# Kernel optimization log

Measured on AMD Instinct MI355X. Metric: run time of the kernel, lower is better.

## Reference

```python
import jax, jax.numpy as jnp
import numpy as np

DIM = 384
HEADS = 12
WS = (7, 7, 7)
N = WS[0] * WS[1] * WS[2]  # 343
NW = 64   # number of windows (mask dim)
B_ = 64   # num_windows * batch
CPB_HIDDEN = 512


def _make_buffers():
    # relative coords table: (1, 2Wd-1, 2Wh-1, 2Ww-1, 3), log-spaced per Swin-V2
    axes = [np.arange(-(w - 1), w, dtype=np.float32) / (w - 1) for w in WS]
    g = np.stack(np.meshgrid(*axes, indexing='ij'), axis=-1)[None]  # (1,13,13,13,3)
    g = g * 8.0
    table = np.sign(g) * np.log2(np.abs(g) + 1.0) / np.log2(8.0)
    # relative position index: (N, N) int
    coords = np.stack(np.meshgrid(*[np.arange(w) for w in WS], indexing='ij'))  # (3,Wd,Wh,Ww)
    cf = coords.reshape(3, -1)
    rel = (cf[:, :, None] - cf[:, None, :]).transpose(1, 2, 0).astype(np.int64)  # (N,N,3)
    rel[..., 0] += WS[0] - 1
    rel[..., 1] += WS[1] - 1
    rel[..., 2] += WS[2] - 1
    rel[..., 0] *= (2 * WS[1] - 1) * (2 * WS[2] - 1)
    rel[..., 1] *= 2 * WS[2] - 1
    idx = rel.sum(-1)
    return jnp.asarray(table, dtype=jnp.float32), jnp.asarray(idx, dtype=jnp.int32)


def setup_inputs() -> dict:
    key = jax.random.key(0)
    ks = jax.random.split(key, 10)
    table, idx = _make_buffers()
    return {
        'x': jax.random.normal(ks[0], (B_, N, DIM), dtype=jnp.float32),
        'mask': jax.random.normal(ks[1], (NW, N, N), dtype=jnp.float32),
        'qkv_w': jax.random.normal(ks[2], (3 * DIM, DIM), dtype=jnp.float32) * 0.02,
        'q_bias': jax.random.normal(ks[3], (DIM,), dtype=jnp.float32) * 0.02,
        'v_bias': jax.random.normal(ks[4], (DIM,), dtype=jnp.float32) * 0.02,
        'logit_scale': jnp.log(10.0 * jnp.ones((HEADS, 1, 1), dtype=jnp.float32)),
        'cpb_w1': jax.random.normal(ks[5], (CPB_HIDDEN, 3), dtype=jnp.float32) * 0.02,
        'cpb_b1': jax.random.normal(ks[6], (CPB_HIDDEN,), dtype=jnp.float32) * 0.02,
        'cpb_w2': jax.random.normal(ks[7], (HEADS, CPB_HIDDEN), dtype=jnp.float32) * 0.02,
        'proj_w': jax.random.normal(ks[8], (DIM, DIM), dtype=jnp.float32) * 0.02,
        'proj_b': jax.random.normal(ks[9], (DIM,), dtype=jnp.float32) * 0.02,
        'rel_table': table,
        'rel_index': idx,
    }


def reference(x, mask, qkv_w, q_bias, v_bias, logit_scale, cpb_w1, cpb_b1,
              cpb_w2, proj_w, proj_b, rel_table, rel_index):
    Bw, n, C = x.shape
    H = logit_scale.shape[0]
    hd = C // H
    qkv_bias = jnp.concatenate([q_bias, jnp.zeros_like(v_bias), v_bias])
    qkv = x @ qkv_w.T + qkv_bias                      # (Bw, n, 3C)
    qkv = qkv.reshape(Bw, n, 3, H, hd).transpose(2, 0, 3, 1, 4)
    q, k, v = qkv[0], qkv[1], qkv[2]                  # (Bw, H, n, hd)
    qn = q / jnp.clip(jnp.linalg.norm(q, axis=-1, keepdims=True), 1e-12)
    kn = k / jnp.clip(jnp.linalg.norm(k, axis=-1, keepdims=True), 1e-12)
    attn = jnp.einsum('bhnd,bhmd->bhnm', qn, kn)
    scale = jnp.exp(jnp.minimum(logit_scale, jnp.log(100.0)))  # clamp max log(1/0.01)
    attn = attn * scale
    # CPB MLP bias: (1,13,13,13,3) -> (table_size, H), gathered to (H, n, n)
    hidden = jax.nn.relu(rel_table @ cpb_w1.T + cpb_b1)
    bias_table = (hidden @ cpb_w2.T).reshape(-1, H)
    bias = bias_table[rel_index.reshape(-1)].reshape(n, n, H).transpose(2, 0, 1)
    bias = 16.0 * jax.nn.sigmoid(bias)
    attn = attn + bias[None]
    nW = mask.shape[0]
    attn = attn.reshape(Bw // nW, nW, H, n, n) + mask[None, :, None]
    attn = attn.reshape(Bw, H, n, n)
    attn = jax.nn.softmax(attn, axis=-1)
    out = jnp.einsum('bhnm,bhmd->bnhd', attn, v).reshape(Bw, n, C)
    out = out @ proj_w.T + proj_b
    return out
```

## Files before the change

### kernel.cpp

```cpp
#include <hip/hip_runtime.h>
#include <hip/hip_bf16.h>
#include <stdint.h>


typedef __attribute__((ext_vector_type(4))) float f32x4;
typedef __attribute__((ext_vector_type(8))) short short8;

#define DIM   384
#define HEADS 12
#define NTOK  343
#define NPAD  352
#define BW    64
#define MROWS (BW*NTOK)
#define MPAD  22016
#define NN    (NTOK*NTOK)
#define BPAD  352
#define LOG2E 1.44269504089f

__device__ __forceinline__ unsigned short f2bf(float f) {
  unsigned u = __float_as_uint(f);
  u += 0x7FFF + ((u >> 16) & 1);
  return (unsigned short)(u >> 16);
}

__device__ __forceinline__ void gload_lds16(const void* g, void* l) {
  __builtin_amdgcn_global_load_lds(
      (const __attribute__((address_space(1))) void*)g,
      (__attribute__((address_space(3))) void*)l, 16, 0, 0);
}

__global__ __launch_bounds__(256) void cvt_bf16(const float* __restrict__ in,
                                                unsigned short* __restrict__ out,
                                                long nvalid, long ntotal) {
  long i = ((long)blockIdx.x * 256 + threadIdx.x) * 8;
  if (i >= ntotal) return;
  short8 o;
  if (i < nvalid) {
    const float4* p = (const float4*)(in + i);
    float4 a = p[0], b = p[1];
    o[0] = (short)f2bf(a.x); o[1] = (short)f2bf(a.y);
    o[2] = (short)f2bf(a.z); o[3] = (short)f2bf(a.w);
    o[4] = (short)f2bf(b.x); o[5] = (short)f2bf(b.y);
    o[6] = (short)f2bf(b.z); o[7] = (short)f2bf(b.w);
  } else {
    o = (short8)0;
  }
  *(short8*)(out + i) = o;
}

__global__ __launch_bounds__(64) void cpb_tab(const float* __restrict__ tbl,
                                              const float* __restrict__ w1,
                                              const float* __restrict__ b1,
                                              const float* __restrict__ w2,
                                              float* __restrict__ btab) {
  const int r = blockIdx.x, lane = threadIdx.x;
  const float t0 = tbl[r*3], t1 = tbl[r*3+1], t2 = tbl[r*3+2];
  float acc[12];
#pragma unroll
  for (int hh = 0; hh < 12; ++hh) acc[hh] = 0.f;
  for (int u = 0; u < 8; ++u) {
    const int j = lane * 8 + u;
    const float hd = fmaxf(w1[j*3]*t0 + w1[j*3+1]*t1 + w1[j*3+2]*t2 + b1[j], 0.f);
#pragma unroll
    for (int hh = 0; hh < 12; ++hh) acc[hh] += hd * w2[hh*512 + j];
  }
#pragma unroll
  for (int hh = 0; hh < 12; ++hh) {
    float v = acc[hh];
    for (int msk = 1; msk < 64; msk <<= 1) v += __shfl_xor(v, msk);
    if (lane == 0) btab[r*12 + hh] = v;
  }
}

__global__ __launch_bounds__(256) void bias_gather(const float* __restrict__ btab,
                                                   const int* __restrict__ ridx,
                                                   float* __restrict__ bfull) {
  const int blk = blockIdx.x;
  const int hh = blk / NTOK, i = blk % NTOK;
  for (int j = threadIdx.x; j < BPAD; j += 256) {
    float o = 0.f;
    if (j < NTOK) {
      const int idx = ridx[i*NTOK + j];
      const float v = btab[idx*12 + hh];
      o = LOG2E * 16.f / (1.f + __expf(-v));
    }
    bfull[(size_t)blk*BPAD + j] = o;
  }
}

template<int MODE>
__global__ __launch_bounds__(256, 2) void gemm_k(
    const unsigned short* __restrict__ A, const unsigned short* __restrict__ B,
    unsigned short* __restrict__ o_qn, unsigned short* __restrict__ o_kn,
    unsigned short* __restrict__ o_vT,
    const float* __restrict__ q_bias, const float* __restrict__ v_bias,
    const float* __restrict__ lsc,
    float* __restrict__ o_out, const float* __restrict__ proj_b) {
  __shared__ alignas(16) uint8_t lds[32768];
  const int tid = threadIdx.x, wave = tid >> 6, lane = tid & 63;
  const int row0 = blockIdx.x * 128, col0 = blockIdx.y * 128;
  const int wm = wave & 1, wn = wave >> 1;
  const int l15 = lane & 15, lq = lane >> 4;
  f32x4 acc[4][4];
#pragma unroll
  for (int i = 0; i < 4; ++i)
#pragma unroll
    for (int j = 0; j < 4; ++j) acc[i][j] = (f32x4)0.f;

  const int stg_row = wave * 8 + (lane >> 3);
  const int srcblk = (lane & 7) ^ (lane >> 3);

  for (int kt = 0; kt < 6; ++kt) {
    const int k0 = kt * 64;
#pragma unroll
    for (int c = 0; c < 4; ++c) {
      const int row = c * 32 + stg_row;
      gload_lds16(A + (size_t)(row0 + row) * DIM + k0 + srcblk * 8,
                  lds + c * 4096 + wave * 1024);
      gload_lds16(B + (size_t)(col0 + row) * DIM + k0 + srcblk * 8,
                  lds + 16384 + c * 4096 + wave * 1024);
    }
    __syncthreads();
#pragma unroll
    for (int s = 0; s < 2; ++s) {
      short8 af[4], bfr[4];
#pragma unroll
      for (int i = 0; i < 4; ++i) {
        const int r = wm * 64 + i * 16 + l15;
        af[i] = *(const short8*)(lds + r * 128 + (((s * 4) | lq) ^ (r & 7)) * 16);
        const int cc = wn * 64 + i * 16 + l15;
        bfr[i] = *(const short8*)(lds + 16384 + cc * 128 + (((s * 4) | lq) ^ (cc & 7)) * 16);
      }
#pragma unroll
      for (int i = 0; i < 4; ++i)
#pragma unroll
        for (int j = 0; j < 4; ++j)
          acc[i][j] = __builtin_amdgcn_mfma_f32_16x16x32_bf16(af[i], bfr[j], acc[i][j], 0, 0, 0);
    }
    __syncthreads();
  }

  if (MODE == 0) {
#pragma unroll
    for (int i = 0; i < 4; ++i) {
      const int gr0 = row0 + wm * 64 + i * 16 + lq * 4;
#pragma unroll
      for (int p = 0; p < 2; ++p) {
        f32x4 c0 = acc[i][2 * p], c1 = acc[i][2 * p + 1];
        const int gcb = col0 + wn * 64 + p * 32;
        const int which = gcb / DIM, rem = gcb % DIM, hh = rem / 32;
        float b0 = 0.f, b1 = 0.f;
        if (which == 0) { b0 = q_bias[rem + l15]; b1 = q_bias[rem + l15 + 16]; }
        else if (which == 2) { b0 = v_bias[rem + l15]; b1 = v_bias[rem + l15 + 16]; }
#pragma unroll
        for (int r = 0; r < 4; ++r) { c0[r] += b0; c1[r] += b1; }
        float mult[4] = {1.f, 1.f, 1.f, 1.f};
        if (which < 2) {
          f32x4 ss;
#pragma unroll
          for (int r = 0; r < 4; ++r) ss[r] = c0[r] * c0[r] + c1[r] * c1[r];
#pragma unroll
          for (int msk = 1; msk < 16; msk <<= 1) {
#pragma unroll
            for (int r = 0; r < 4; ++r) ss[r] += __shfl_xor(ss[r], msk);
          }
          float sc = 1.f;
          if (which == 0)
            sc = __expf(fminf(lsc[hh], 4.6051701860f)) * LOG2E;
#pragma unroll
          for (int r = 0; r < 4; ++r) mult[r] = sc / fmaxf(sqrtf(ss[r]), 1e-12f);
        }
#pragma unroll
        for (int r = 0; r < 4; ++r) {
          const int gr = gr0 + r;
          if (gr >= MROWS) continue;
          const int b = gr / NTOK, nt = gr % NTOK;
          const unsigned short v0 = f2bf(c0[r] * mult[r]);
          const unsigned short v1 = f2bf(c1[r] * mult[r]);
          if (which == 0) {
            const size_t base = ((size_t)(b * HEADS + hh) * NTOK + nt) * 32 + l15;
            o_qn[base] = v0; o_qn[base + 16] = v1;
          } else if (which == 1) {
            const size_t base = ((size_t)(b * HEADS + hh) * NTOK + nt) * 32 + l15;
            o_kn[base] = v0; o_kn[base + 16] = v1;
          } else {
            const size_t base = ((size_t)(b * HEADS + hh) * 32 + l15) * NPAD + nt;
            o_vT[base] = v0; o_vT[base + (size_t)16 * NPAD] = v1;
          }
        }
      }
    }
  } else {
#pragma unroll
    for (int i = 0; i < 4; ++i) {
      const int gr0 = row0 + wm * 64 + i * 16 + lq * 4;
#pragma unroll
      for (int j = 0; j < 4; ++j) {
        const int gc = col0 + wn * 64 + j * 16 + l15;
        const float pb = proj_b[gc];
#pragma unroll
        for (int r = 0; r < 4; ++r) {
          const int gr = gr0 + r;
          if (gr < MROWS) o_out[(size_t)gr * DIM + gc] = acc[i][j][r] + pb;
        }
      }
    }
  }
}

__global__ __launch_bounds__(256, 3) void attn_k(
    const unsigned short* __restrict__ qn, const unsigned short* __restrict__ kn,
    const unsigned short* __restrict__ vT, const float* __restrict__ bfull,
    const float* __restrict__ mask, unsigned short* __restrict__ out1) {
  __shared__ alignas(16) uint8_t lds[33280];
  const int g = blockIdx.x;
  const int b = (g & 7) * 8 + (g >> 3) / HEADS;
  const int hh = (g >> 3) % HEADS;
  const int bh = b * HEADS + hh;
  const int tid = threadIdx.x;

  for (int r = tid; r < NPAD; r += 256) {
    uint4* dst = (uint4*)(lds + r * 80);
    if (r < NTOK) {
      const uint4* src = (const uint4*)(kn + ((size_t)bh * NTOK + r) * 32);
      dst[0] = src[0]; dst[1] = src[1]; dst[2] = src[2]; dst[3] = src[3];
    } else {
      uint4 z = make_uint4(0, 0, 0, 0);
      dst[0] = z; dst[1] = z; dst[2] = z; dst[3] = z;
    }
  }
  __syncthreads();

  const int wave = tid >> 6, lane = tid & 63;
  const int l15 = lane & 15, lq = lane >> 4;
  uint8_t* pbuf = lds + 28160 + wave * 1280;

  const unsigned short* vrow0 = vT + ((size_t)bh * 32 + l15) * NPAD;
  const unsigned short* vrow1 = vT + ((size_t)bh * 32 + 16 + l15) * NPAD;

  for (int qt = wave; qt < 22; qt += 4) {
    const int q0 = qt * 16;
    const int qc = min(q0 + l15, NTOK - 1);
    const short8 aq = *(const short8*)(qn + ((size_t)bh * NTOK + qc) * 32 + lq * 8);
    const float* brow = bfull + ((size_t)hh * NTOK + qc) * BPAD;
    const float* mrow = mask + (size_t)b * NN + (size_t)qc * NTOK;

    f32x4 o0 = (f32x4)0.f, o1 = (f32x4)0.f;
    float m_run = -1e30f, l_run = 0.f;

    f32x4 pf_ba[2], pf_bb[2];
    float pf_ma[2][4], pf_mb[2][4];
    short8 pf_v0[2], pf_v1[2], pf_k0[2], pf_k1[2];

    pf_ba[0] = *(const f32x4*)(brow + lq * 4);
    pf_bb[0] = *(const f32x4*)(brow + 16 + lq * 4);
#pragma unroll
    for (int r = 0; r < 4; ++r) {
      pf_ma[0][r] = mrow[lq * 4 + r];
      pf_mb[0][r] = mrow[16 + lq * 4 + r];
    }
    pf_v0[0] = *(const short8*)(vrow0 + lq * 8);
    pf_v1[0] = *(const short8*)(vrow1 + lq * 8);
    pf_k0[0] = *(const short8*)(lds + (l15) * 80 + lq * 16);
    pf_k1[0] = *(const short8*)(lds + (16 + l15) * 80 + lq * 16);

#pragma unroll
    for (int c = 0; c < 11; ++c) {
      const int cur = c & 1, nxt = cur ^ 1;
      if (c < 10) {
        const int kc = (c + 1) * 32;
        pf_ba[nxt] = *(const f32x4*)(brow + kc + lq * 4);
        pf_bb[nxt] = *(const f32x4*)(brow + kc + 16 + lq * 4);
#pragma unroll
        for (int r = 0; r < 4; ++r) {
          pf_ma[nxt][r] = mrow[kc + lq * 4 + r];
          const int kk = kc + 16 + lq * 4 + r;
          pf_mb[nxt][r] = mrow[(c == 9 && kk >= NTOK) ? 0 : kk];
        }
        pf_v0[nxt] = *(const short8*)(vrow0 + kc + lq * 8);
        pf_v1[nxt] = *(const short8*)(vrow1 + kc + lq * 8);
        pf_k0[nxt] = *(const short8*)(lds + (kc + l15) * 80 + lq * 16);
        pf_k1[nxt] = *(const short8*)(lds + (kc + 16 + l15) * 80 + lq * 16);
      }
      f32x4 s0 = __builtin_amdgcn_mfma_f32_16x16x32_bf16(pf_k0[cur], aq, (f32x4)0.f, 0, 0, 0);
      f32x4 s1 = __builtin_amdgcn_mfma_f32_16x16x32_bf16(pf_k1[cur], aq, (f32x4)0.f, 0, 0, 0);
#pragma unroll
      for (int r = 0; r < 4; ++r) {
        s0[r] = s0[r] + pf_ba[cur][r] + pf_ma[cur][r] * LOG2E;
        s1[r] = s1[r] + pf_bb[cur][r] + pf_mb[cur][r] * LOG2E;
      }
      if (c == 10) {
#pragma unroll
        for (int r = 0; r < 4; ++r)
          if (336 + lq * 4 + r >= NTOK) s1[r] = -1e30f;
      }
      float mx = fmaxf(fmaxf(fmaxf(s0[0], s0[1]), fmaxf(s0[2], s0[3])),
                       fmaxf(fmaxf(s1[0], s1[1]), fmaxf(s1[2], s1[3])));
      mx = fmaxf(mx, __shfl_xor(mx, 16));
      mx = fmaxf(mx, __shfl_xor(mx, 32));
      const float mn = fmaxf(m_run, mx);
      const float f = exp2f(m_run - mn);
      m_run = mn;
      float p0[4], p1[4], psum = 0.f;
#pragma unroll
      for (int r = 0; r < 4; ++r) {
        p0[r] = exp2f(s0[r] - mn);
        p1[r] = exp2f(s1[r] - mn);
        psum += p0[r] + p1[r];
      }
      l_run = l_run * f + psum;
      float fr[4];
#pragma unroll
      for (int r = 0; r < 4; ++r) fr[r] = __shfl(f, lq * 4 + r);
#pragma unroll
      for (int r = 0; r < 4; ++r) { o0[r] *= fr[r]; o1[r] *= fr[r]; }
      const unsigned uu0 = ((unsigned)f2bf(p0[1]) << 16) | f2bf(p0[0]);
      const unsigned uu1 = ((unsigned)f2bf(p0[3]) << 16) | f2bf(p0[2]);
      const unsigned uu2 = ((unsigned)f2bf(p1[1]) << 16) | f2bf(p1[0]);
      const unsigned uu3 = ((unsigned)f2bf(p1[3]) << 16) | f2bf(p1[2]);
      uint2* w0 = (uint2*)(pbuf + l15 * 80 + lq * 8);
      uint2* w1 = (uint2*)(pbuf + l15 * 80 + 32 + lq * 8);
      *w0 = make_uint2(uu0, uu1);
      *w1 = make_uint2(uu2, uu3);
      const short8 pfrag = *(const short8*)(pbuf + l15 * 80 + lq * 16);
      o0 = __builtin_amdgcn_mfma_f32_16x16x32_bf16(pfrag, pf_v0[cur], o0, 0, 0, 0);
      o1 = __builtin_amdgcn_mfma_f32_16x16x32_bf16(pfrag, pf_v1[cur], o1, 0, 0, 0);
    }
    l_run += __shfl_xor(l_run, 16);
    l_run += __shfl_xor(l_run, 32);
    const float invl = 1.f / l_run;
    float ir[4];
#pragma unroll
    for (int r = 0; r < 4; ++r) ir[r] = __shfl(invl, lq * 4 + r);
#pragma unroll
    for (int r = 0; r < 4; ++r) {
      const int q = q0 + lq * 4 + r;
      if (q < NTOK) {
        const size_t base = ((size_t)b * NTOK + q) * DIM + hh * 32 + l15;
        out1[base]      = f2bf(o0[r] * ir[r]);
        out1[base + 16] = f2bf(o1[r] * ir[r]);
      }
    }
  }
}

extern "C" void kernel_launch(void* const* d_in, const int* in_sizes, int n_in,
                              void* d_out, int out_size, void* d_ws, size_t ws_size,
                              hipStream_t stream) {
  const float* x      = (const float*)d_in[0];
  const float* mask   = (const float*)d_in[1];
  const float* qkv_w  = (const float*)d_in[2];
  const float* q_bias = (const float*)d_in[3];
  const float* v_bias = (const float*)d_in[4];
  const float* lsc    = (const float*)d_in[5];
  const float* cpb_w1 = (const float*)d_in[6];
  const float* cpb_b1 = (const float*)d_in[7];
  const float* cpb_w2 = (const float*)d_in[8];
  const float* proj_w = (const float*)d_in[9];
  const float* proj_b = (const float*)d_in[10];
  const float* rtab   = (const float*)d_in[11];
  const int*   ridx   = (const int*)d_in[12];
  float* out = (float*)d_out;
  uint8_t* ws = (uint8_t*)d_ws;

  size_t o = 0;
  auto alloc = [&](size_t bytes) { size_t r = o; o += (bytes + 255) & ~(size_t)255; return r; };
  const size_t off_xb  = alloc((size_t)MPAD * DIM * 2);
  const size_t off_qwb = alloc((size_t)1152 * DIM * 2);
  const size_t off_pwb = alloc((size_t)DIM * DIM * 2);
  const size_t off_qnb = alloc((size_t)BW * HEADS * NTOK * 32 * 2);
  const size_t off_knb = alloc((size_t)BW * HEADS * NTOK * 32 * 2);
  const size_t off_vTb = alloc((size_t)BW * HEADS * 32 * NPAD * 2);
  const size_t off_btab  = alloc((size_t)2197 * 12 * 4);
  const size_t off_bfull = alloc((size_t)HEADS * NTOK * BPAD * 4);
  (void)in_sizes; (void)n_in; (void)out_size;

  if (ws_size < o) {
    hipMemsetAsync(d_out, 0, (size_t)out_size * 4, stream);
    return;
  }

  unsigned short* xb  = (unsigned short*)(ws + off_xb);
  unsigned short* o1b = xb;
  unsigned short* qwb = (unsigned short*)(ws + off_qwb);
  unsigned short* pwb = (unsigned short*)(ws + off_pwb);
  unsigned short* qnb = (unsigned short*)(ws + off_qnb);
  unsigned short* knb = (unsigned short*)(ws + off_knb);
  unsigned short* vTb = (unsigned short*)(ws + off_vTb);
  float* btab  = (float*)(ws + off_btab);
  float* bfull = (float*)(ws + off_bfull);

  cvt_bf16<<<(long)MPAD * DIM / 8 / 256, 256, 0, stream>>>(x, xb, (long)MROWS * DIM, (long)MPAD * DIM);
  cvt_bf16<<<1152 * DIM / 8 / 256, 256, 0, stream>>>(qkv_w, qwb, 1152L * DIM, 1152L * DIM);
  cvt_bf16<<<DIM * DIM / 8 / 256, 256, 0, stream>>>(proj_w, pwb, (long)DIM * DIM, (long)DIM * DIM);
  cpb_tab<<<2197, 64, 0, stream>>>(rtab, cpb_w1, cpb_b1, cpb_w2, btab);
  bias_gather<<<HEADS * NTOK, 256, 0, stream>>>(btab, ridx, bfull);
  gemm_k<0><<<dim3(MPAD / 128, 1152 / 128), 256, 0, stream>>>(
      xb, qwb, qnb, knb, vTb, q_bias, v_bias, lsc, nullptr, nullptr);
  attn_k<<<BW * HEADS, 256, 0, stream>>>(qnb, knb, vTb, bfull, mask, o1b);
  gemm_k<1><<<dim3(MPAD / 128, DIM / 128), 256, 0, stream>>>(
      o1b, pwb, nullptr, nullptr, nullptr, nullptr, nullptr, nullptr, out, proj_b);
}
```

Baseline: 310.6 us.

## Replace online softmax with fixed-max exponent, split query tiles across two blocks

The attention kernel drops the running-max online softmax. It relies on a static upper bound: the cosine logits are bounded by the clamped scale, the bias is at most 16, and the shift SMAX is folded into the gathered bias table, so the exponent is computed directly without max reductions, shuffles or accumulator rescaling. Padding columns are masked through a -1e9 bias entry instead of a separate branch. Each (window, head) is split across two blocks to double the grid, occupancy is raised to 4 blocks per CU, and the P·V MFMA is software-pipelined one chunk behind using a double P buffer. Bf16 packing switches to truncation instead of round-to-nearest. The fixed max assumes the mask values are bounded; large mask values could overflow or underflow exp2.

```diff
diff --git a/kernel.cpp b/kernel.cpp
--- a/kernel.cpp
+++ b/kernel.cpp
@@ -16,11 +16,16 @@
 #define NN    (NTOK*NTOK)
 #define BPAD  352
 #define LOG2E 1.44269504089f
+#define SMAX  48.0f
 
 __device__ __forceinline__ unsigned short f2bf(float f) {
   unsigned u = __float_as_uint(f);
   u += 0x7FFF + ((u >> 16) & 1);
   return (unsigned short)(u >> 16);
+}
+
+__device__ __forceinline__ unsigned pk2bf(float lo, float hi) {
+  return (__float_as_uint(hi) & 0xFFFF0000u) | (__float_as_uint(lo) >> 16);
 }
 
 __device__ __forceinline__ void gload_lds16(const void* g, void* l) {
@@ -78,11 +83,11 @@
   const int blk = blockIdx.x;
   const int hh = blk / NTOK, i = blk % NTOK;
   for (int j = threadIdx.x; j < BPAD; j += 256) {
-    float o = 0.f;
+    float o = -1e9f;
     if (j < NTOK) {
       const int idx = ridx[i*NTOK + j];
       const float v = btab[idx*12 + hh];
-      o = LOG2E * 16.f / (1.f + __expf(-v));
+      o = LOG2E * 16.f / (1.f + __expf(-v)) - SMAX;
     }
     bfull[(size_t)blk*BPAD + j] = o;
   }
@@ -208,14 +213,16 @@
   }
 }
 
-__global__ __launch_bounds__(256, 3) void attn_k(
+__global__ __launch_bounds__(256, 4) void attn_k(
     const unsigned short* __restrict__ qn, const unsigned short* __restrict__ kn,
     const unsigned short* __restrict__ vT, const float* __restrict__ bfull,
     const float* __restrict__ mask, unsigned short* __restrict__ out1) {
-  __shared__ alignas(16) uint8_t lds[33280];
+  __shared__ alignas(16) uint8_t lds[38400];
   const int g = blockIdx.x;
-  const int b = (g & 7) * 8 + (g >> 3) / HEADS;
-  const int hh = (g >> 3) % HEADS;
+  const int idx = g >> 3;
+  const int b = (g & 7) * 8 + idx / 24;
+  const int r24 = idx % 24;
+  const int hh = r24 >> 1, half = r24 & 1;
   const int bh = b * HEADS + hh;
   const int tid = threadIdx.x;
 
@@ -233,98 +240,78 @@
 
   const int wave = tid >> 6, lane = tid & 63;
   const int l15 = lane & 15, lq = lane >> 4;
-  uint8_t* pbuf = lds + 28160 + wave * 1280;
+  uint8_t* pb0 = lds + 28160 + wave * 2560;
+  uint8_t* pb1 = pb0 + 1280;
 
   const unsigned short* vrow0 = vT + ((size_t)bh * 32 + l15) * NPAD;
   const unsigned short* vrow1 = vT + ((size_t)bh * 32 + 16 + l15) * NPAD;
 
-  for (int qt = wave; qt < 22; qt += 4) {
-    const int q0 = qt * 16;
+  for (int t = wave; t < 11; t += 4) {
+    const int q0 = (half * 11 + t) * 16;
     const int qc = min(q0 + l15, NTOK - 1);
     const short8 aq = *(const short8*)(qn + ((size_t)bh * NTOK + qc) * 32 + lq * 8);
     const float* brow = bfull + ((size_t)hh * NTOK + qc) * BPAD;
     const float* mrow = mask + (size_t)b * NN + (size_t)qc * NTOK;
 
     f32x4 o0 = (f32x4)0.f, o1 = (f32x4)0.f;
-    float m_run = -1e30f, l_run = 0.f;
-
-    f32x4 pf_ba[2], pf_bb[2];
-    float pf_ma[2][4], pf_mb[2][4];
-    short8 pf_v0[2], pf_v1[2], pf_k0[2], pf_k1[2];
-
-    pf_ba[0] = *(const f32x4*)(brow + lq * 4);
-    pf_bb[0] = *(const f32x4*)(brow + 16 + lq * 4);
+    float l_run = 0.f;
+
+    f32x4 pbA[2], pbB[2];
+    float pmA[2][4], pmB[2][4];
+    short8 kf0[2], kf1[2], vf0[2], vf1[2];
+
+    pbA[0] = *(const f32x4*)(brow + lq * 4);
+    pbB[0] = *(const f32x4*)(brow + 16 + lq * 4);
 #pragma unroll
     for (int r = 0; r < 4; ++r) {
-      pf_ma[0][r] = mrow[lq * 4 + r];
-      pf_mb[0][r] = mrow[16 + lq * 4 + r];
-    }
-    pf_v0[0] = *(const short8*)(vrow0 + lq * 8);
-    pf_v1[0] = *(const short8*)(vrow1 + lq * 8);
-    pf_k0[0] = *(const short8*)(lds + (l15) * 80 + lq * 16);
-    pf_k1[0] = *(const short8*)(lds + (16 + l15) * 80 + lq * 16);
-
-#pragma unroll
-    for (int c = 0; c < 11; ++c) {
+      pmA[0][r] = mrow[lq * 4 + r];
+      pmB[0][r] = mrow[16 + lq * 4 + r];
+    }
+    kf0[0] = *(const short8*)(lds + l15 * 80 + lq * 16);
+    kf1[0] = *(const short8*)(lds + (16 + l15) * 80 + lq * 16);
+
+#pragma unroll
+    for (int c = 0; c <= 10; ++c) {
       const int cur = c & 1, nxt = cur ^ 1;
+      const int kc = c * 32;
+      vf0[cur] = *(const short8*)(vrow0 + kc + lq * 8);
+      vf1[cur] = *(const short8*)(vrow1 + kc + lq * 8);
       if (c < 10) {
-        const int kc = (c + 1) * 32;
-        pf_ba[nxt] = *(const f32x4*)(brow + kc + lq * 4);
-        pf_bb[nxt] = *(const f32x4*)(brow + kc + 16 + lq * 4);
+        const int k2 = kc + 32;
+        pbA[nxt] = *(const f32x4*)(brow + k2 + lq * 4);
+        pbB[nxt] = *(const f32x4*)(brow + k2 + 16 + lq * 4);
 #pragma unroll
         for (int r = 0; r < 4; ++r) {
-          pf_ma[nxt][r] = mrow[kc + lq * 4 + r];
-          const int kk = kc + 16 + lq * 4 + r;
-          pf_mb[nxt][r] = mrow[(c == 9 && kk >= NTOK) ? 0 : kk];
+          pmA[nxt][r] = mrow[k2 + lq * 4 + r];
+          const int kk = k2 + 16 + lq * 4 + r;
+          pmB[nxt][r] = mrow[(c == 9 && kk >= NTOK) ? 0 : kk];
         }
-        pf_v0[nxt] = *(const short8*)(vrow0 + kc + lq * 8);
-        pf_v1[nxt] = *(const short8*)(vrow1 + kc + lq * 8);
-        pf_k0[nxt] = *(const short8*)(lds + (kc + l15) * 80 + lq * 16);
-        pf_k1[nxt] = *(const short8*)(lds + (kc + 16 + l15) * 80 + lq * 16);
-      }
-      f32x4 s0 = __builtin_amdgcn_mfma_f32_16x16x32_bf16(pf_k0[cur], aq, (f32x4)0.f, 0, 0, 0);
-      f32x4 s1 = __builtin_amdgcn_mfma_f32_16x16x32_bf16(pf_k1[cur], aq, (f32x4)0.f, 0, 0, 0);
+        kf0[nxt] = *(const short8*)(lds + (k2 + l15) * 80 + lq * 16);
+        kf1[nxt] = *(const short8*)(lds + (k2 + 16 + l15) * 80 + lq * 16);
+      }
+      f32x4 s0 = __builtin_amdgcn_mfma_f32_16x16x32_bf16(kf0[cur], aq, (f32x4)0.f, 0, 0, 0);
+      f32x4 s1 = __builtin_amdgcn_mfma_f32_16x16x32_bf16(kf1[cur], aq, (f32x4)0.f, 0, 0, 0);
+      float p0[4], p1[4], ps = 0.f;
 #pragma unroll
       for (int r = 0; r < 4; ++r) {
-        s0[r] = s0[r] + pf_ba[cur][r] + pf_ma[cur][r] * LOG2E;
-        s1[r] = s1[r] + pf_bb[cur][r] + pf_mb[cur][r] * LOG2E;
-      }
-      if (c == 10) {
-#pragma unroll
-        for (int r = 0; r < 4; ++r)
-          if (336 + lq * 4 + r >= NTOK) s1[r] = -1e30f;
-      }
-      float mx = fmaxf(fmaxf(fmaxf(s0[0], s0[1]), fmaxf(s0[2], s0[3])),
-                       fmaxf(fmaxf(s1[0], s1[1]), fmaxf(s1[2], s1[3])));
-      mx = fmaxf(mx, __shfl_xor(mx, 16));
-      mx = fmaxf(mx, __shfl_xor(mx, 32));
-      const float mn = fmaxf(m_run, mx);
-      const float f = exp2f(m_run - mn);
-      m_run = mn;
-      float p0[4], p1[4], psum = 0.f;
-#pragma unroll
-      for (int r = 0; r < 4; ++r) {
-        p0[r] = exp2f(s0[r] - mn);
-        p1[r] = exp2f(s1[r] - mn);
-        psum += p0[r] + p1[r];
-      }
-      l_run = l_run * f + psum;
-      float fr[4];
-#pragma unroll
-      for (int r = 0; r < 4; ++r) fr[r] = __shfl(f, lq * 4 + r);
-#pragma unroll
-      for (int r = 0; r < 4; ++r) { o0[r] *= fr[r]; o1[r] *= fr[r]; }
-      const unsigned uu0 = ((unsigned)f2bf(p0[1]) << 16) | f2bf(p0[0]);
-      const unsigned uu1 = ((unsigned)f2bf(p0[3]) << 16) | f2bf(p0[2]);
-      const unsigned uu2 = ((unsigned)f2bf(p1[1]) << 16) | f2bf(p1[0]);
-      const unsigned uu3 = ((unsigned)f2bf(p1[3]) << 16) | f2bf(p1[2]);
-      uint2* w0 = (uint2*)(pbuf + l15 * 80 + lq * 8);
-      uint2* w1 = (uint2*)(pbuf + l15 * 80 + 32 + lq * 8);
-      *w0 = make_uint2(uu0, uu1);
-      *w1 = make_uint2(uu2, uu3);
-      const short8 pfrag = *(const short8*)(pbuf + l15 * 80 + lq * 16);
-      o0 = __builtin_amdgcn_mfma_f32_16x16x32_bf16(pfrag, pf_v0[cur], o0, 0, 0, 0);
-      o1 = __builtin_amdgcn_mfma_f32_16x16x32_bf16(pfrag, pf_v1[cur], o1, 0, 0, 0);
+        p0[r] = exp2f(s0[r] + fmaf(pmA[cur][r], LOG2E, pbA[cur][r]));
+        p1[r] = exp2f(s1[r] + fmaf(pmB[cur][r], LOG2E, pbB[cur][r]));
+        ps += p0[r] + p1[r];
+      }
+      l_run += ps;
+      uint8_t* pw = (cur ? pb1 : pb0) + l15 * 80;
+      *(uint2*)(pw + lq * 8)      = make_uint2(pk2bf(p0[0], p0[1]), pk2bf(p0[2], p0[3]));
+      *(uint2*)(pw + 32 + lq * 8) = make_uint2(pk2bf(p1[0], p1[1]), pk2bf(p1[2], p1[3]));
+      if (c > 0) {
+        const short8 pf = *(const short8*)((nxt ? pb1 : pb0) + l15 * 80 + lq * 16);
+        o0 = __builtin_amdgcn_mfma_f32_16x16x32_bf16(pf, vf0[nxt], o0, 0, 0, 0);
+        o1 = __builtin_amdgcn_mfma_f32_16x16x32_bf16(pf, vf1[nxt], o1, 0, 0, 0);
+      }
+    }
+    {
+      const short8 pf = *(const short8*)(pb0 + l15 * 80 + lq * 16);
+      o0 = __builtin_amdgcn_mfma_f32_16x16x32_bf16(pf, vf0[0], o0, 0, 0, 0);
+      o1 = __builtin_amdgcn_mfma_f32_16x16x32_bf16(pf, vf1[0], o1, 0, 0, 0);
     }
     l_run += __shfl_xor(l_run, 16);
     l_run += __shfl_xor(l_run, 32);
@@ -397,7 +384,7 @@
   bias_gather<<<HEADS * NTOK, 256, 0, stream>>>(btab, ridx, bfull);
   gemm_k<0><<<dim3(MPAD / 128, 1152 / 128), 256, 0, stream>>>(
       xb, qwb, qnb, knb, vTb, q_bias, v_bias, lsc, nullptr, nullptr);
-  attn_k<<<BW * HEADS, 256, 0, stream>>>(qnb, knb, vTb, bfull, mask, o1b);
+  attn_k<<<2 * BW * HEADS, 256, 0, stream>>>(qnb, knb, vTb, bfull, mask, o1b);
   gemm_k<1><<<dim3(MPAD / 128, DIM / 128), 256, 0, stream>>>(
       o1b, pwb, nullptr, nullptr, nullptr, nullptr, nullptr, nullptr, out, proj_b);
 }
```

Measured after the change: 356.0 us. +14.6%, slower.
